# Kernel tuning notes

Measured on AMD Instinct MI355X. Metric: run time of the kernel, lower is better.

Reference implementation:

```python
import jax, jax.numpy as jnp
import numpy as np

N, C, H, W = 4, 128, 64, 64


def setup_inputs() -> dict:
    key = jax.random.key(0)
    ks = jax.random.split(key, 4)
    s = 1.0 / np.sqrt(C).astype(np.float32)  # conv2d default-init scale
    return {
        "x": jax.random.normal(ks[0], (N, C, H, W), dtype=jnp.float32),
        "Wq": jax.random.normal(ks[1], (C, C), dtype=jnp.float32) * s,
        "bq": jnp.zeros((C,), dtype=jnp.float32),
        "Wk": jax.random.normal(ks[2], (C, C), dtype=jnp.float32) * s,
        "bk": jnp.zeros((C,), dtype=jnp.float32),
        "Wv": jax.random.normal(ks[3], (C, C), dtype=jnp.float32) * s,
        "bv": jnp.zeros((C,), dtype=jnp.float32),
    }


def reference(x, Wq, bq, Wk, bk, Wv, bv):
    n, c, h, w = x.shape
    xf = x.reshape(n, c, h * w)  # [N, C, L], L = H*W
    # 1x1 convs == per-pixel channel mixing
    q = jnp.einsum('oc,ncl->nol', Wq, xf) + bq[:, None]
    k = jnp.einsum('oc,ncl->nol', Wk, xf) + bk[:, None]
    v = jnp.einsum('oc,ncl->nol', Wv, xf) + bv[:, None]
    # scores[l, m] = sum_c k[c,l] * q[c,m]  (matmul(k^T, q))
    scale = jnp.asarray(1.0 / np.sqrt(c), x.dtype)
    scores = jnp.einsum('ncl,ncm->nlm', k, q) * scale  # [N, L, L]
    temp = jax.nn.softmax(scores, axis=-1)
    attn = jnp.einsum('ncl,nlm->ncm', v, temp)  # [N, C, L]
    return x + attn.reshape(n, c, h, w)
```

## Files before the change

### kernel.cpp

```cpp
#include <hip/hip_runtime.h>
#include <hip/hip_bf16.h>
#include <stdint.h>

#define NB 4
#define CH 128
#define LL 4096

typedef __attribute__((ext_vector_type(8))) short short8;
typedef __attribute__((ext_vector_type(4))) short short4b;
typedef __attribute__((ext_vector_type(4))) float floatx4;
typedef __attribute__((ext_vector_type(16))) float floatx16;


static __device__ __forceinline__ short f2bf(float f) {
    uint32_t u = __float_as_uint(f);
    u += 0x7fffu + ((u >> 16) & 1u);
    return (short)(u >> 16);
}
static __device__ __forceinline__ float bf2f(short s) {
    return __uint_as_float(((uint32_t)(uint16_t)s) << 16);
}

__global__ __launch_bounds__(256) void wprep_kernel(
    const float* __restrict__ Wq, const float* __restrict__ Wk,
    const float* __restrict__ Wv, short* __restrict__ Wf)
{
    const int g = blockIdx.x * 256 + threadIdx.x;
    const int mat = g >> 14;
    const int rem = g & 16383;
    const int o   = rem >> 7;
    const int c   = rem & 127;
    const float* W = (mat == 0) ? Wq : (mat == 1) ? Wk : Wv;
    float v = W[o * CH + c];
    if (mat == 1) v *= 0.08838834764831845f;
    Wf[(size_t)mat * 16384 + (o >> 4) * 2048 + (c >> 5) * 512
       + ((c >> 3) & 3) * 128 + (o & 15) * 8 + (c & 7)] = f2bf(v);
}

__global__ __launch_bounds__(256) void proj_kernel(
    const float* __restrict__ x, const short* __restrict__ Wf,
    const float* __restrict__ bq, const float* __restrict__ bk,
    const float* __restrict__ bv,
    short* __restrict__ Qf, short* __restrict__ Kf, short* __restrict__ Vp)
{
    const int b    = blockIdx.x;
    const int n    = b >> 7;
    const int lt   = b & 127;
    const int l0   = lt << 5;
    const int tid  = threadIdx.x;
    const int wave = tid >> 6;
    const int lane = tid & 63;
    const int quad = lane >> 4;
    const int mc   = lane & 15;

    __shared__ short Xb[32][136];

    {
        const int sl = tid & 31;
        const int cg = tid >> 5;
        const float* xp = x + ((size_t)n * CH + cg * 16) * LL + l0 + sl;
        short8 buf;
        #pragma unroll
        for (int i = 0; i < 16; ++i) {
            buf[i & 7] = f2bf(xp[(size_t)i * LL]);
            if ((i & 7) == 7)
                *(short8*)(void*)&Xb[sl][cg * 16 + (i & 8)] = buf;
        }
    }
    __syncthreads();

    const int lt2 = wave >> 1;
    const int oh  = wave & 1;
    const int gt  = lt * 2 + lt2;

    short8 xf[4];
    #pragma unroll
    for (int s = 0; s < 4; ++s)
        xf[s] = *(const short8*)(const void*)&Xb[lt2 * 16 + mc][32 * s + quad * 8];

    const size_t obase = ((size_t)n * 256 + gt) * 2048;
    const float scale = 0.08838834764831845f;

    #pragma unroll
    for (int mat = 0; mat < 3; ++mat) {
        const short* Wm = Wf + (size_t)mat * 16384;
        const float* bb = (mat == 0) ? bq : (mat == 1) ? bk : bv;
        const float bscale = (mat == 1) ? scale : 1.0f;
        #pragma unroll
        for (int ot = oh * 4; ot < oh * 4 + 4; ++ot) {
            floatx4 acc = {0.f, 0.f, 0.f, 0.f};
            #pragma unroll
            for (int s = 0; s < 4; ++s)
                acc = __builtin_amdgcn_mfma_f32_16x16x32_bf16(
                    *(const short8*)(const void*)(Wm + ot * 2048 + s * 512 + lane * 8),
                    xf[s], acc, 0, 0, 0);
            const int c0 = ot * 16 + 4 * quad;
            if (mat < 2) {
                short4b pv;
                #pragma unroll
                for (int r = 0; r < 4; ++r)
                    pv[r] = f2bf(acc[r] + bb[c0 + r] * bscale);
                short* dst = ((mat == 0) ? Qf : Kf) + obase
                           + (c0 >> 5) * 512 + ((c0 >> 3) & 3) * 128
                           + mc * 8 + (c0 & 7);
                *(short4b*)(void*)dst = pv;
            } else {
                #pragma unroll
                for (int r = 0; r < 4; ++r)
                    Vp[obase + (c0 + r) * 16 + mc] = f2bf(acc[r] + bb[c0 + r]);
            }
        }
    }
}

__global__ __launch_bounds__(256) void rowsum_kernel(
    const short* __restrict__ Qf, const short* __restrict__ Kf,
    const short* __restrict__ Vp, short* __restrict__ Vs)
{
    const int b    = blockIdx.x;
    const int n    = b >> 7;
    const int tp   = b & 127;
    const int tid  = threadIdx.x;
    const int wave = tid >> 6;
    const int lane = tid & 63;
    const int quad = lane >> 4;
    const int mc   = lane & 15;

    __shared__ float Db[4][32];
    __shared__ float Dr[32];

    const short* Kb = Kf + ((size_t)n * 256 + tp * 2) * 2048 + lane * 8;
    short8 kf[2][4];
    #pragma unroll
    for (int t = 0; t < 2; ++t)
        #pragma unroll
        for (int s = 0; s < 4; ++s)
            kf[t][s] = *(const short8*)(const void*)(Kb + t * 2048 + s * 512);

    const short* Qn = Qf + (size_t)n * 524288 + (size_t)wave * 64 * 2048 + lane * 8;
    float rs[2][4] = {{0.f,0.f,0.f,0.f},{0.f,0.f,0.f,0.f}};

    for (int i = 0; i < 64; i += 2) {
        floatx4 a[2][2];
        #pragma unroll
        for (int t = 0; t < 2; ++t)
            #pragma unroll
            for (int j = 0; j < 2; ++j) a[t][j] = (floatx4){0.f,0.f,0.f,0.f};
        #pragma unroll
        for (int s = 0; s < 4; ++s) {
            const short8 q0 = *(const short8*)(const void*)(Qn + (size_t)i * 2048 + s * 512);
            const short8 q1 = *(const short8*)(const void*)(Qn + (size_t)(i + 1) * 2048 + s * 512);
            #pragma unroll
            for (int t = 0; t < 2; ++t) {
                a[t][0] = __builtin_amdgcn_mfma_f32_16x16x32_bf16(kf[t][s], q0, a[t][0], 0, 0, 0);
                a[t][1] = __builtin_amdgcn_mfma_f32_16x16x32_bf16(kf[t][s], q1, a[t][1], 0, 0, 0);
            }
        }
        #pragma unroll
        for (int t = 0; t < 2; ++t)
            #pragma unroll
            for (int j = 0; j < 2; ++j)
                #pragma unroll
                for (int r = 0; r < 4; ++r) rs[t][r] += __expf(a[t][j][r]);
    }

    #pragma unroll
    for (int t = 0; t < 2; ++t) {
        #pragma unroll
        for (int r = 0; r < 4; ++r) {
            float v = rs[t][r];
            v += __shfl_xor(v, 1);
            v += __shfl_xor(v, 2);
            v += __shfl_xor(v, 4);
            v += __shfl_xor(v, 8);
            rs[t][r] = v;
        }
        if (mc == 0) {
            #pragma unroll
            for (int r = 0; r < 4; ++r)
                Db[wave][t * 16 + quad * 4 + r] = rs[t][r];
        }
    }
    __syncthreads();
    if (tid < 32)
        Dr[tid] = 1.0f / (Db[0][tid] + Db[1][tid] + Db[2][tid] + Db[3][tid]);
    __syncthreads();

    const short* vsrc = Vp + ((size_t)n * 256 + tp * 2) * 2048;
    short*       vdst = Vs + ((size_t)n * 256 + tp * 2) * 2048;
    #pragma unroll
    for (int k = 0; k < 16; ++k) {
        const int i = k * 256 + tid;
        const int tile = i >> 11;
        const int li   = i & 15;
        vdst[i] = f2bf(bf2f(vsrc[i]) * Dr[tile * 16 + li]);
    }
}

__global__ __launch_bounds__(1024) void attn_out_kernel(
    const short* __restrict__ Qf, const short* __restrict__ Kf,
    const short* __restrict__ Vs,
    const float* __restrict__ x, float* __restrict__ out)
{
    const int b    = blockIdx.x;
    const int n    = b >> 6;
    const int m0   = (b & 63) << 6;
    const int tid  = threadIdx.x;
    const int wave = tid >> 6;
    const int lane = tid & 63;
    const int quad = lane >> 4;
    const int mc   = lane & 15;
    const int l32  = lane & 31;
    const int h    = lane >> 5;
    const int ct   = wave & 3;
    const int mh   = (wave >> 2) & 1;
    const int kh   = wave >> 3;

    __shared__ short P[2][64][264];
    __shared__ float Rbuf[4][2][64][16];

    const short* Qn  = Qf + (size_t)n * 524288;
    const short* Kn  = Kf + (size_t)n * 524288;
    const short* Vpn = Vs + (size_t)n * 524288;

    short8 qf[4][4];
    #pragma unroll
    for (int mst = 0; mst < 4; ++mst)
        #pragma unroll
        for (int s = 0; s < 4; ++s)
            qf[mst][s] = *(const short8*)(const void*)(
                Qn + (size_t)((m0 >> 4) + mst) * 2048 + s * 512 + lane * 8);

    floatx16 acc;
    #pragma unroll
    for (int r = 0; r < 16; ++r) acc[r] = 0.f;

    for (int step = 0; step < 16; ++step) {
        const int lb = step << 8;
        const int p  = step & 1;

        short8 kfr[4];
        #pragma unroll
        for (int s = 0; s < 4; ++s)
            kfr[s] = *(const short8*)(const void*)(
                Kn + (size_t)(step * 16 + wave) * 2048 + s * 512 + lane * 8);

        #pragma unroll
        for (int mst = 0; mst < 4; ++mst) {
            floatx4 sa = {0.f, 0.f, 0.f, 0.f};
            #pragma unroll
            for (int s = 0; s < 4; ++s)
                sa = __builtin_amdgcn_mfma_f32_16x16x32_bf16(kfr[s], qf[mst][s], sa, 0, 0, 0);
            short4b pv;
            #pragma unroll
            for (int r = 0; r < 4; ++r) pv[r] = f2bf(__expf(sa[r]));
            *(short4b*)(void*)&P[p][16 * mst + mc][16 * wave + quad * 4] = pv;
        }
        __syncthreads();

        #pragma unroll
        for (int i = 0; i < 8; ++i) {
            const int kc = kh * 8 + i;
            const short8 vf = *(const short8*)(const void*)(
                Vpn + (size_t)((lb >> 4) + kc) * 2048 + (32 * ct + l32) * 16 + 8 * h);
            const short8 pf = *(const short8*)(const void*)&P[p][32 * mh + l32][16 * kc + 8 * h];
            acc = __builtin_amdgcn_mfma_f32_32x32x16_bf16(vf, pf, acc, 0, 0, 0);
        }
    }

    __syncthreads();
    if (kh == 1)
        *(floatx16*)(void*)&Rbuf[ct][mh][lane][0] = acc;
    __syncthreads();
    if (kh == 0) {
        const floatx16 o = *(const floatx16*)(const void*)&Rbuf[ct][mh][lane][0];
        #pragma unroll
        for (int r = 0; r < 16; ++r) {
            const int c = 32 * ct + (r & 3) + 8 * (r >> 2) + 4 * h;
            const int m = m0 + 32 * mh + l32;
            const size_t idx = ((size_t)n * CH + c) * LL + m;
            out[idx] = x[idx] + acc[r] + o[r];
        }
    }
}

extern "C" void kernel_launch(void* const* d_in, const int* in_sizes, int n_in,
                              void* d_out, int out_size, void* d_ws, size_t ws_size,
                              hipStream_t stream) {
    (void)in_sizes; (void)n_in; (void)out_size; (void)ws_size;
    const float* x  = (const float*)d_in[0];
    const float* Wq = (const float*)d_in[1];
    const float* bq = (const float*)d_in[2];
    const float* Wk = (const float*)d_in[3];
    const float* bk = (const float*)d_in[4];
    const float* Wv = (const float*)d_in[5];
    const float* bv = (const float*)d_in[6];
    float* out = (float*)d_out;

    char* ws = (char*)d_ws;
    short* Qf = (short*)(ws);
    short* Kf = (short*)(ws + 4194304);
    short* Vp = (short*)(ws + 8388608);
    short* Vs = (short*)(ws + 12582912);
    short* Wf = (short*)(ws + 16777216);

    wprep_kernel<<<192, 256, 0, stream>>>(Wq, Wk, Wv, Wf);
    proj_kernel<<<512, 256, 0, stream>>>(x, Wf, bq, bk, bv, Qf, Kf, Vp);
    rowsum_kernel<<<512, 256, 0, stream>>>(Qf, Kf, Vp, Vs);
    attn_out_kernel<<<256, 1024, 0, stream>>>(Qf, Kf, Vs, x, out);
}
```

Baseline: 166.9 us.

## Apply softmax normalization in attention kernel instead of rescaling V

The rowsum kernel now writes only reciprocal row sums to a small float buffer instead of producing a rescaled bf16 copy of V. The attention kernel multiplies each exp score by the matching reciprocal before storing P. The rowsum kernel also moves to 1024-thread blocks covering 64 rows each and double-buffers Q fragment loads in registers. This removes a full read and write of V and moves the normalization multiply into the inner loop of the attention kernel, where it adds a small per-step load.

After: 167.7 us. No clear change (+0.5%).

```diff
diff --git a/kernel.cpp b/kernel.cpp
--- a/kernel.cpp
+++ b/kernel.cpp
@@ -113,23 +113,24 @@
     }
 }
 
-__global__ __launch_bounds__(256) void rowsum_kernel(
+__global__ __launch_bounds__(1024) void rowsum_kernel(
     const short* __restrict__ Qf, const short* __restrict__ Kf,
-    const short* __restrict__ Vp, short* __restrict__ Vs)
+    float* __restrict__ Dv)
 {
     const int b    = blockIdx.x;
-    const int n    = b >> 7;
-    const int tp   = b & 127;
+    const int n    = b >> 6;
+    const int tq   = b & 63;
     const int tid  = threadIdx.x;
     const int wave = tid >> 6;
     const int lane = tid & 63;
     const int quad = lane >> 4;
     const int mc   = lane & 15;
-
-    __shared__ float Db[4][32];
-    __shared__ float Dr[32];
-
-    const short* Kb = Kf + ((size_t)n * 256 + tp * 2) * 2048 + lane * 8;
+    const int mw   = wave & 7;
+    const int th   = wave >> 3;
+
+    __shared__ float Db[16][32];
+
+    const short* Kb = Kf + ((size_t)n * 256 + tq * 4 + th * 2) * 2048 + lane * 8;
     short8 kf[2][4];
     #pragma unroll
     for (int t = 0; t < 2; ++t)
@@ -137,35 +138,44 @@
         for (int s = 0; s < 4; ++s)
             kf[t][s] = *(const short8*)(const void*)(Kb + t * 2048 + s * 512);
 
-    const short* Qn = Qf + (size_t)n * 524288 + (size_t)wave * 64 * 2048 + lane * 8;
-    float rs[2][4] = {{0.f,0.f,0.f,0.f},{0.f,0.f,0.f,0.f}};
-
-    for (int i = 0; i < 64; i += 2) {
-        floatx4 a[2][2];
-        #pragma unroll
-        for (int t = 0; t < 2; ++t)
-            #pragma unroll
-            for (int j = 0; j < 2; ++j) a[t][j] = (floatx4){0.f,0.f,0.f,0.f};
+    const short* Qn = Qf + (size_t)n * 524288 + (size_t)mw * 32 * 2048 + lane * 8;
+    float rs[2][4] = {{0.f, 0.f, 0.f, 0.f}, {0.f, 0.f, 0.f, 0.f}};
+
+    short8 qA[4], qB[4];
+    #pragma unroll
+    for (int s = 0; s < 4; ++s)
+        qA[s] = *(const short8*)(const void*)(Qn + s * 512);
+
+    auto qstep = [&](const short8 (&q)[4]) {
+        floatx4 a0 = {0.f, 0.f, 0.f, 0.f};
+        floatx4 a1 = {0.f, 0.f, 0.f, 0.f};
         #pragma unroll
         for (int s = 0; s < 4; ++s) {
-            const short8 q0 = *(const short8*)(const void*)(Qn + (size_t)i * 2048 + s * 512);
-            const short8 q1 = *(const short8*)(const void*)(Qn + (size_t)(i + 1) * 2048 + s * 512);
-            #pragma unroll
-            for (int t = 0; t < 2; ++t) {
-                a[t][0] = __builtin_amdgcn_mfma_f32_16x16x32_bf16(kf[t][s], q0, a[t][0], 0, 0, 0);
-                a[t][1] = __builtin_amdgcn_mfma_f32_16x16x32_bf16(kf[t][s], q1, a[t][1], 0, 0, 0);
-            }
-        }
-        #pragma unroll
-        for (int t = 0; t < 2; ++t)
-            #pragma unroll
-            for (int j = 0; j < 2; ++j)
-                #pragma unroll
-                for (int r = 0; r < 4; ++r) rs[t][r] += __expf(a[t][j][r]);
-    }
-
-    #pragma unroll
-    for (int t = 0; t < 2; ++t) {
+            a0 = __builtin_amdgcn_mfma_f32_16x16x32_bf16(kf[0][s], q[s], a0, 0, 0, 0);
+            a1 = __builtin_amdgcn_mfma_f32_16x16x32_bf16(kf[1][s], q[s], a1, 0, 0, 0);
+        }
+        #pragma unroll
+        for (int r = 0; r < 4; ++r) {
+            rs[0][r] += __expf(a0[r]);
+            rs[1][r] += __expf(a1[r]);
+        }
+    };
+
+    for (int it = 0; it < 32; it += 2) {
+        #pragma unroll
+        for (int s = 0; s < 4; ++s)
+            qB[s] = *(const short8*)(const void*)(
+                Qn + (size_t)((it + 1) & 31) * 2048 + s * 512);
+        qstep(qA);
+        #pragma unroll
+        for (int s = 0; s < 4; ++s)
+            qA[s] = *(const short8*)(const void*)(
+                Qn + (size_t)((it + 2) & 31) * 2048 + s * 512);
+        qstep(qB);
+    }
+
+    #pragma unroll
+    for (int t = 0; t < 2; ++t)
         #pragma unroll
         for (int r = 0; r < 4; ++r) {
             float v = rs[t][r];
@@ -173,33 +183,21 @@
             v += __shfl_xor(v, 2);
             v += __shfl_xor(v, 4);
             v += __shfl_xor(v, 8);
-            rs[t][r] = v;
-        }
-        if (mc == 0) {
-            #pragma unroll
-            for (int r = 0; r < 4; ++r)
-                Db[wave][t * 16 + quad * 4 + r] = rs[t][r];
-        }
-    }
+            if (mc == 0) Db[wave][t * 16 + quad * 4 + r] = v;
+        }
     __syncthreads();
-    if (tid < 32)
-        Dr[tid] = 1.0f / (Db[0][tid] + Db[1][tid] + Db[2][tid] + Db[3][tid]);
-    __syncthreads();
-
-    const short* vsrc = Vp + ((size_t)n * 256 + tp * 2) * 2048;
-    short*       vdst = Vs + ((size_t)n * 256 + tp * 2) * 2048;
-    #pragma unroll
-    for (int k = 0; k < 16; ++k) {
-        const int i = k * 256 + tid;
-        const int tile = i >> 11;
-        const int li   = i & 15;
-        vdst[i] = f2bf(bf2f(vsrc[i]) * Dr[tile * 16 + li]);
+    if (tid < 64) {
+        const int lh = tid >> 5, lr = tid & 31;
+        float s = 0.f;
+        #pragma unroll
+        for (int m = 0; m < 8; ++m) s += Db[lh * 8 + m][lr];
+        Dv[(size_t)n * 4096 + tq * 64 + tid] = 1.0f / s;
     }
 }
 
 __global__ __launch_bounds__(1024) void attn_out_kernel(
     const short* __restrict__ Qf, const short* __restrict__ Kf,
-    const short* __restrict__ Vs,
+    const short* __restrict__ Vp, const float* __restrict__ Dv,
     const float* __restrict__ x, float* __restrict__ out)
 {
     const int b    = blockIdx.x;
@@ -221,7 +219,8 @@
 
     const short* Qn  = Qf + (size_t)n * 524288;
     const short* Kn  = Kf + (size_t)n * 524288;
-    const short* Vpn = Vs + (size_t)n * 524288;
+    const short* Vpn = Vp + (size_t)n * 524288;
+    const float* Dn  = Dv + (size_t)n * 4096;
 
     short8 qf[4][4];
     #pragma unroll
@@ -244,6 +243,8 @@
         for (int s = 0; s < 4; ++s)
             kfr[s] = *(const short8*)(const void*)(
                 Kn + (size_t)(step * 16 + wave) * 2048 + s * 512 + lane * 8);
+        const floatx4 dr = *(const floatx4*)(const void*)(
+            Dn + lb + wave * 16 + quad * 4);
 
         #pragma unroll
         for (int mst = 0; mst < 4; ++mst) {
@@ -253,7 +254,7 @@
                 sa = __builtin_amdgcn_mfma_f32_16x16x32_bf16(kfr[s], qf[mst][s], sa, 0, 0, 0);
             short4b pv;
             #pragma unroll
-            for (int r = 0; r < 4; ++r) pv[r] = f2bf(__expf(sa[r]));
+            for (int r = 0; r < 4; ++r) pv[r] = f2bf(__expf(sa[r]) * dr[r]);
             *(short4b*)(void*)&P[p][16 * mst + mc][16 * wave + quad * 4] = pv;
         }
         __syncthreads();
@@ -301,11 +302,11 @@
     short* Qf = (short*)(ws);
     short* Kf = (short*)(ws + 4194304);
     short* Vp = (short*)(ws + 8388608);
-    short* Vs = (short*)(ws + 12582912);
+    float* Dv = (float*)(ws + 12582912);
     short* Wf = (short*)(ws + 16777216);
 
     wprep_kernel<<<192, 256, 0, stream>>>(Wq, Wk, Wv, Wf);
     proj_kernel<<<512, 256, 0, stream>>>(x, Wf, bq, bk, bv, Qf, Kf, Vp);
-    rowsum_kernel<<<512, 256, 0, stream>>>(Qf, Kf, Vp, Vs);
-    attn_out_kernel<<<256, 1024, 0, stream>>>(Qf, Kf, Vs, x, out);
-}
+    rowsum_kernel<<<256, 1024, 0, stream>>>(Qf, Kf, Dv);
+    attn_out_kernel<<<256, 1024, 0, stream>>>(Qf, Kf, Vp, Dv, x, out);
+}
```
